# Performance work log

Measured on AMD Instinct MI355X. Metric: run time of the kernel, lower is better.

## Reference

```python
import jax, jax.numpy as jnp
import numpy as np

# Model config (matches init_kwargs)
D_MODEL = 512
D_STATE = 64
D_CONV = 4
EXPAND = 2
NHEADS = 16
HEADDIM = 64
D_INNER = EXPAND * D_MODEL          # 1024 == NHEADS * HEADDIM
D_IN_PROJ = 2 * D_INNER + 2 * D_STATE + NHEADS  # 2192
BATCH = 2
SEQLEN = 2048


def setup_inputs() -> dict:
    key = jax.random.key(0)
    ks = jax.random.split(key, 5)
    s = 0.02  # weight scale so activations stay well-conditioned
    return {
        "x": jax.random.normal(ks[0], (BATCH, SEQLEN, D_MODEL), jnp.float32),
        "W_in": jax.random.normal(ks[1], (D_IN_PROJ, D_MODEL), jnp.float32) * s,
        "conv_w": jax.random.normal(ks[2], (D_INNER, 1, D_CONV), jnp.float32) * 0.3,
        "conv_b": jnp.zeros((D_INNER,), jnp.float32),
        "A_log": jnp.zeros((NHEADS,), jnp.float32),       # torch init: log(ones)=0
        "dt_bias": jnp.ones((NHEADS,), jnp.float32),
        "W_out": jax.random.normal(ks[3], (D_MODEL, D_INNER), jnp.float32) * s,
    }


def reference(x, W_in, conv_w, conv_b, A_log, dt_bias, W_out):
    b, l, _ = x.shape
    # in_proj (no bias)
    proj = jnp.einsum('bld,ed->ble', x, W_in)  # [b, l, D_IN_PROJ]
    z, xs, B, C, dt = jnp.split(
        proj, [D_INNER, 2 * D_INNER, 2 * D_INNER + D_STATE, 2 * D_INNER + 2 * D_STATE], axis=-1)

    # depthwise causal conv1d: torch pads (d_conv-1) on both sides then truncates
    # right to seqlen, equivalent to left-padding by d_conv-1.
    xc = jax.lax.conv_general_dilated(
        xs.transpose(0, 2, 1), conv_w,
        window_strides=(1,), padding=[(D_CONV - 1, 0)],
        dimension_numbers=('NCH', 'OIH', 'NCH'),
        feature_group_count=D_INNER)
    xc = xc + conv_b[None, :, None]
    x_ssm = jax.nn.silu(xc).transpose(0, 2, 1)           # [b, l, D_INNER]
    xh = x_ssm.reshape(b, l, NHEADS, HEADDIM)            # [b, l, h, p]

    dt = jax.nn.softplus(dt + dt_bias)                   # [b, l, h]
    A = -jnp.exp(A_log)                                  # [h]
    dA = jnp.exp(dt * A)                                 # [b, l, h], in (0,1)

    # sequential selective scan over time (lax.scan), state h: [b, h, n, p]
    def step(h, inp):
        dAt, Bt, Ct, xt = inp                            # [b,h],[b,n],[b,n],[b,h,p]
        h = dAt[:, :, None, None] * h + jnp.einsum('bn,bhp->bhnp', Bt, xt)
        y = jnp.einsum('bn,bhnp->bhp', Ct, h)
        return h, y

    h0 = jnp.zeros((b, NHEADS, D_STATE, HEADDIM), x.dtype)
    _, ys = jax.lax.scan(step, h0, (dA.transpose(1, 0, 2),
                                    B.transpose(1, 0, 2),
                                    C.transpose(1, 0, 2),
                                    xh.transpose(1, 0, 2, 3)))
    y = ys.transpose(1, 0, 2, 3).reshape(b, l, D_INNER)  # [b, l, d_inner]

    y = y * jax.nn.silu(z)                               # gated output
    return jnp.einsum('ble,de->bld', y, W_out)           # out_proj (no bias)
```

## Files before the change

### kernel.cpp

```cpp
#include <hip/hip_runtime.h>
#include <cstdint>
#include <cstddef>

#define B_N     2
#define L_N     2048
#define DMODEL  512
#define DINNER  1024
#define DSTATE  64
#define NHEADS  16
#define EPROJ   2192
#define PB      2176
#define OFF_Z   0
#define OFF_XP  1024
#define OFF_B   2048
#define OFF_C   2112
#define LC      64
#define NC      32
#define MROWS   4096

typedef unsigned short u16;
typedef unsigned int   u32;
typedef __attribute__((ext_vector_type(8))) short short8;
typedef __attribute__((ext_vector_type(4))) float floatx4;

__device__ __forceinline__ float silu_f(float v) { return v / (1.f + __expf(-v)); }

__device__ __forceinline__ u16 f2bf(float f) {
    union { float f; uint32_t u; } v; v.f = f;
    uint32_t r = (v.u + 0x7FFFu + ((v.u >> 16) & 1u)) >> 16;
    return (u16)r;
}

__device__ __forceinline__ float bf2f(u16 b) {
    union { u32 u; float f; } v; v.u = (u32)b << 16; return v.f;
}

__device__ __forceinline__ u32 pack2(float lo, float hi) {
    return (u32)f2bf(lo) | ((u32)f2bf(hi) << 16);
}

__device__ __forceinline__ u32 cvtpk(float lo, float hi) {
    u32 r;
    asm("v_cvt_pk_bf16_f32 %0, %1, %2" : "=v"(r) : "v"(lo), "v"(hi));
    return r;
}

__device__ __forceinline__ uint4 pk8(const float4& a, const float4& b) {
    uint4 o;
    o.x = cvtpk(a.x, a.y); o.y = cvtpk(a.z, a.w);
    o.z = cvtpk(b.x, b.y); o.w = cvtpk(b.z, b.w);
    return o;
}

__device__ __forceinline__ float lane_bcast(float v, int n) {
    union { float f; uint32_t u; } a, b;
    a.f = v;
    b.u = __builtin_amdgcn_readlane(a.u, n);
    return b.f;
}

__device__ __forceinline__ short8 frag_ld(const u32* s, int row, int k0) {
    const u32* q = s + row * 33 + (k0 >> 1);
    union { u32 u[4]; short8 v; } r;
    r.u[0] = q[0]; r.u[1] = q[1]; r.u[2] = q[2]; r.u[3] = q[3];
    return r.v;
}

__device__ __forceinline__ void gload_lds16(const u16* g, u16* s) {
    __builtin_amdgcn_global_load_lds(
        (const __attribute__((address_space(1))) void*)g,
        (__attribute__((address_space(3))) void*)s,
        16, 0, 0);
}

template<int BM, int BN, int NPB, bool GUARD, bool PSPLIT, bool CVTIN,
         int NBX, int RBX, int RBY>
__global__ __launch_bounds__(256, 2) void gemm_mfma_bt(
    const void* __restrict__ Av, const void* __restrict__ Btv,
    float* __restrict__ Cf, u16* __restrict__ Cb, float* __restrict__ Dt,
    int M, int N, int K)
{
    constexpr int MI = BM / 32;
    constexpr int NI = BN / 32;
    constexpr int KB = 32 * NPB;
    constexpr int NGA = BM / 64;
    constexpr int NGB = (BN / 16 + 3) / 4;
    constexpr int XC  = NBX / RBX;
    __shared__ u16 As_[2][NPB][BM * 32];
    __shared__ u16 Bs_[2][NPB][BN * 32];

    const int tid = threadIdx.x;
    const int w   = tid >> 6;
    const int ln  = tid & 63;
    const int wm  = w >> 1, wn = w & 1;

    const int k  = blockIdx.x & 7;
    const int j  = blockIdx.x >> 3;
    const int bx = (k % XC) * RBX + (j % RBX);
    const int by = (k / XC) * RBY + (j / RBX);
    const int bm = by * BM;
    const int bn = bx * BN;

    const int srow = ln >> 2;
    const int skq  = (ln & 3) * 8;
    const int fr = ln & 15;
    const int fq = (ln >> 4) * 8;

    floatx4 acc[MI][NI];
    const floatx4 fzero = {0.f, 0.f, 0.f, 0.f};
    #pragma unroll
    for (int mi = 0; mi < MI; ++mi)
        #pragma unroll
        for (int ni = 0; ni < NI; ++ni) acc[mi][ni] = fzero;

    auto compute = [&](int buf) {
        #pragma unroll
        for (int p = 0; p < NPB; ++p) {
            short8 af[MI], bfv[NI];
            #pragma unroll
            for (int mi = 0; mi < MI; ++mi)
                af[mi] = *(const short8*)&As_[buf][p][(wm * (BM / 2) + mi * 16 + fr) * 32 + fq];
            #pragma unroll
            for (int ni = 0; ni < NI; ++ni)
                bfv[ni] = *(const short8*)&Bs_[buf][p][(wn * (BN / 2) + ni * 16 + fr) * 32 + fq];
            #pragma unroll
            for (int mi = 0; mi < MI; ++mi)
                #pragma unroll
                for (int ni = 0; ni < NI; ++ni)
                    acc[mi][ni] = __builtin_amdgcn_mfma_f32_16x16x32_bf16(
                        af[mi], bfv[ni], acc[mi][ni], 0, 0, 0);
        }
    };

    if constexpr (CVTIN) {
        const float* A  = (const float*)Av;
        const float* Bt = (const float*)Btv;
        float4 hA[NPB][NGA][2];
        float4 hB[NPB][NGB][2];

        auto ld = [&](int k0) {
            #pragma unroll
            for (int p = 0; p < NPB; ++p) {
                const int kp = k0 + p * 32;
                #pragma unroll
                for (int gi = 0; gi < NGA; ++gi) {
                    const int g = gi * 4 + w;
                    const float* s = A + (size_t)(bm + g * 16 + srow) * K + kp + skq;
                    hA[p][gi][0] = *(const float4*)s;
                    hA[p][gi][1] = *(const float4*)(s + 4);
                }
                #pragma unroll
                for (int gi = 0; gi < NGB; ++gi) {
                    const int g = gi * 4 + w;
                    if (g < BN / 16) {
                        int rn = bn + g * 16 + srow;
                        if (GUARD) rn = (rn < N) ? rn : (N - 1);
                        const float* s = Bt + (size_t)rn * K + kp + skq;
                        hB[p][gi][0] = *(const float4*)s;
                        hB[p][gi][1] = *(const float4*)(s + 4);
                    }
                }
            }
        };
        auto st = [&](int buf) {
            #pragma unroll
            for (int p = 0; p < NPB; ++p) {
                #pragma unroll
                for (int gi = 0; gi < NGA; ++gi) {
                    const int g = gi * 4 + w;
                    ((uint4*)&As_[buf][p][g * 16 * 32])[ln] =
                        pk8(hA[p][gi][0], hA[p][gi][1]);
                }
                #pragma unroll
                for (int gi = 0; gi < NGB; ++gi) {
                    const int g = gi * 4 + w;
                    if (g < BN / 16)
                        ((uint4*)&Bs_[buf][p][g * 16 * 32])[ln] =
                            pk8(hB[p][gi][0], hB[p][gi][1]);
                }
            }
        };

        ld(0); st(0);
        __syncthreads();
        int cur = 0;
        for (int k0 = 0; k0 + KB < K; k0 += KB) {
            ld(k0 + KB);
            compute(cur);
            st(cur ^ 1);
            __syncthreads();
            cur ^= 1;
        }
        compute(cur);
    } else {
        const u16* A  = (const u16*)Av;
        const u16* Bt = (const u16*)Btv;

        auto stage = [&](int buf, int k0) {
            #pragma unroll
            for (int p = 0; p < NPB; ++p) {
                const int kp = k0 + p * 32;
                #pragma unroll
                for (int g = 0; g < BM / 16; ++g) {
                    if ((g & 3) != w) continue;
                    gload_lds16(A + (size_t)(bm + g * 16 + srow) * K + kp + skq,
                                &As_[buf][p][g * 16 * 32]);
                }
                #pragma unroll
                for (int g = 0; g < BN / 16; ++g) {
                    if ((g & 3) != w) continue;
                    int rn = bn + g * 16 + srow;
                    if (GUARD) rn = (rn < N) ? rn : (N - 1);
                    gload_lds16(Bt + (size_t)rn * K + kp + skq,
                                &Bs_[buf][p][g * 16 * 32]);
                }
            }
        };

        stage(0, 0);
        __syncthreads();
        int cur = 0;
        for (int k0 = 0; k0 + KB < K; k0 += KB) {
            stage(cur ^ 1, k0 + KB);
            compute(cur);
            __syncthreads();
            cur ^= 1;
        }
        compute(cur);
    }

    const int cr = (ln >> 4) * 4;
    const int cc = ln & 15;
    #pragma unroll
    for (int mi = 0; mi < MI; ++mi) {
        const int row0 = bm + wm * (BM / 2) + mi * 16 + cr;
        #pragma unroll
        for (int ni = 0; ni < NI; ++ni) {
            const int col = bn + wn * (BN / 2) + ni * 16 + cc;
            #pragma unroll
            for (int r = 0; r < 4; ++r) {
                const int row = row0 + r;
                const float v = acc[mi][ni][r];
                if (PSPLIT) {
                    if (col < PB)
                        Cb[(size_t)row * PB + col] = f2bf(v);
                    else if (col < EPROJ)
                        Dt[(size_t)(col - PB) * MROWS + row] = v;
                } else {
                    Cf[(size_t)row * N + col] = v;
                }
            }
        }
    }
}

__global__ __launch_bounds__(256) void ssd_phase1(
    const u16* __restrict__ projb, const float* __restrict__ dtf,
    const float* __restrict__ cw, const float* __restrict__ cb,
    const float* __restrict__ A_log, const float* __restrict__ dt_bias,
    u16* __restrict__ hb, float* __restrict__ Pc, float* __restrict__ LaBuf,
    u32* __restrict__ xT)
{
    __shared__ u32 sBD[64 * 33];
    __shared__ u32 sXt[64 * 33];

    const int bid = blockIdx.x;
    const int c = bid & (NC - 1);
    const int h = (bid >> 5) & (NHEADS - 1);
    const int b = bid >> 9;
    const int tid = threadIdx.x;
    const int w = tid >> 6, ln = tid & 63;
    const int a = ln & 15, q = ln >> 4;
    const size_t r0 = (size_t)b * L_N + c * LC;

    float dt = dtf[(size_t)h * MROWS + r0 + ln] + dt_bias[h];
    float sp = (dt > 15.f) ? dt : log1pf(__expf(dt));
    float La = sp * (-__expf(A_log[h]));
    #pragma unroll
    for (int d = 1; d < 64; d <<= 1) {
        float up = __shfl_up(La, d, 64);
        if (ln >= d) La += up;
    }
    if (w == 0) LaBuf[(size_t)bid * 64 + ln] = La;
    const float La63 = lane_bcast(La, 63);

    const int ch = h * 64 + ln;
    const float4 w4 = *(const float4*)(cw + ch * 4);
    const float bias = cb[ch];
    const u16* xcol = projb + OFF_XP + ch;
    const size_t bbase = (size_t)b * L_N;

    float xr[3];
    #pragma unroll
    for (int i = 0; i < 3; ++i) {
        const int tl = c * LC + 16 * w - 3 + i;
        xr[i] = (tl >= 0) ? bf2f(xcol[(bbase + tl) * PB]) : 0.f;
    }

    #pragma unroll
    for (int j = 0; j < 8; ++j) {
        const int sp_ = w * 8 + j, s = sp_ * 2;
        const float xa = bf2f(xcol[(r0 + s) * PB]);
        const float xb = bf2f(xcol[(r0 + s + 1) * PB]);
        float a0 = bias, a1 = bias;
        a0 += xr[0] * w4.x; a0 += xr[1] * w4.y; a0 += xr[2] * w4.z; a0 += xa * w4.w;
        a1 += xr[1] * w4.x; a1 += xr[2] * w4.y; a1 += xa * w4.z;   a1 += xb * w4.w;
        xr[0] = xr[2]; xr[1] = xa; xr[2] = xb;
        const float x0 = silu_f(a0), x1 = silu_f(a1);
        const u32 xp = pack2(x0, x1);
        sXt[ln * 33 + sp_] = xp;
        xT[(size_t)bid * 2048 + sp_ * 64 + ln] = xp;
        const float w0 = __expf(La63 - lane_bcast(La, s));
        const float w1 = __expf(La63 - lane_bcast(La, s + 1));
        const float b0 = bf2f(projb[(r0 + s) * PB + OFF_B + ln]) * w0;
        const float b1 = bf2f(projb[(r0 + s + 1) * PB + OFF_B + ln]) * w1;
        sBD[ln * 33 + sp_] = pack2(b0, b1);
    }
    __syncthreads();

    short8 af[2], bf[4][2];
    #pragma unroll
    for (int ks = 0; ks < 2; ++ks)
        af[ks] = frag_ld(sBD, w * 16 + a, ks * 32 + q * 8);
    #pragma unroll
    for (int tn = 0; tn < 4; ++tn)
        #pragma unroll
        for (int ks = 0; ks < 2; ++ks)
            bf[tn][ks] = frag_ld(sXt, tn * 16 + a, ks * 32 + q * 8);

    const floatx4 fzero = {0.f, 0.f, 0.f, 0.f};
    floatx4 acc[4];
    #pragma unroll
    for (int tn = 0; tn < 4; ++tn) {
        acc[tn] = fzero;
        #pragma unroll
        for (int ks = 0; ks < 2; ++ks)
            acc[tn] = __builtin_amdgcn_mfma_f32_16x16x32_bf16(
                af[ks], bf[tn][ks], acc[tn], 0, 0, 0);
    }

    u16* hp = hb + (size_t)bid * 4096;
    #pragma unroll
    for (int tn = 0; tn < 4; ++tn)
        #pragma unroll
        for (int r = 0; r < 4; ++r)
            hp[(w * 16 + q * 4 + r) * 64 + tn * 16 + a] = f2bf(acc[tn][r]);
    if (tid == 0) Pc[bid] = __expf(La63);
}

__global__ __launch_bounds__(256) void ssd_phase2(
    u32* __restrict__ hb32, const float* __restrict__ Pc,
    const float* __restrict__ wsrc, u16* __restrict__ wdst, int nw)
{
    const int bid = blockIdx.x;
    if (bid >= 256) {
        const int i = (bid - 256) * 256 + threadIdx.x;
        if (i < nw) {
            float4 v = ((const float4*)wsrc)[i];
            ushort4 o;
            o.x = f2bf(v.x); o.y = f2bf(v.y); o.z = f2bf(v.z); o.w = f2bf(v.w);
            ((ushort4*)wdst)[i] = o;
        }
        return;
    }

    const int bh = bid >> 3;
    const int e = (bid & 7) * 256 + threadIdx.x;
    const size_t base = (size_t)(bh * NC) * 2048 + e;

    u32 v[NC];
    #pragma unroll
    for (int c = 0; c < NC; ++c)
        v[c] = hb32[base + (size_t)c * 2048];

    float c0 = 0.f, c1 = 0.f;
    #pragma unroll
    for (int c = 0; c < NC; ++c) {
        const u32 cur = v[c];
        const float lo = bf2f((u16)cur), hi = bf2f((u16)(cur >> 16));
        v[c] = pack2(c0, c1);
        const float Pv = Pc[bh * NC + c];
        c0 = fmaf(Pv, c0, lo);
        c1 = fmaf(Pv, c1, hi);
    }

    #pragma unroll
    for (int c = 0; c < NC; ++c)
        hb32[base + (size_t)c * 2048] = v[c];
}

__global__ __launch_bounds__(256) void ssd_phase3(
    const u16* __restrict__ projb, const u32* __restrict__ xT,
    const u16* __restrict__ hb, const float* __restrict__ LaBuf,
    u16* __restrict__ yz)
{
    __shared__ char lds[34048];
    u32* sBW   = (u32*)lds;
    u32* sC    = (u32*)(lds + 8448);
    u32* sXt   = (u32*)(lds + 16896);
    u32* sH    = (u32*)(lds + 25344);
    float* sLaF = (float*)(lds + 33792);
    float* sY  = (float*)(lds + 8448);

    const int bid = blockIdx.x;
    const int c = bid & (NC - 1);
    const int h = (bid >> 5) & (NHEADS - 1);
    const int b = bid >> 9;
    const int tid = threadIdx.x;
    const int w = tid >> 6, ln = tid & 63;
    const int a = ln & 15, q = ln >> 4;
    const int hw = ln >> 5, k32 = ln & 31;
    const size_t r0 = (size_t)b * L_N + c * LC;

    if (tid < 64) sLaF[tid] = LaBuf[(size_t)bid * 64 + tid];

    const u16* hs = hb + (size_t)bid * 4096;
    #pragma unroll
    for (int j = 0; j < 8; ++j) {
        const int rp = w * 8 + j;
        const int row = rp * 2 + hw;
        sBW[row * 33 + k32] = *(const u32*)(projb + (r0 + row) * PB + OFF_B + 2 * k32);
        sC [row * 33 + k32] = *(const u32*)(projb + (r0 + row) * PB + OFF_C + 2 * k32);
        sXt[ln * 33 + rp] = xT[(size_t)bid * 2048 + rp * 64 + ln];
        sH [ln * 33 + rp] = (u32)hs[(2 * rp) * 64 + ln]
                          | ((u32)hs[(2 * rp + 1) * 64 + ln] << 16);
    }
    __syncthreads();

    const floatx4 fzero = {0.f, 0.f, 0.f, 0.f};

    short8 cfr[2], bfr[4][2];
    #pragma unroll
    for (int ks = 0; ks < 2; ++ks)
        cfr[ks] = frag_ld(sC, w * 16 + a, ks * 32 + q * 8);
    #pragma unroll
    for (int tm = 0; tm < 4; ++tm)
        if (tm <= w)
            #pragma unroll
            for (int ks = 0; ks < 2; ++ks)
                bfr[tm][ks] = frag_ld(sBW, tm * 16 + a, ks * 32 + q * 8);
    floatx4 accS[4];
    #pragma unroll
    for (int tm = 0; tm < 4; ++tm) {
        if (tm > w) continue;
        accS[tm] = fzero;
        #pragma unroll
        for (int ks = 0; ks < 2; ++ks)
            accS[tm] = __builtin_amdgcn_mfma_f32_16x16x32_bf16(
                bfr[tm][ks], cfr[ks], accS[tm], 0, 0, 0);
    }
    __syncthreads();

    {
        const int i = w * 16 + a;
        const float Li = sLaF[i];
        #pragma unroll
        for (int tm = 0; tm < 4; ++tm) {
            const int d0 = i * 33 + tm * 8 + q * 2;
            if (tm > w) {
                sBW[d0] = 0; sBW[d0 + 1] = 0;
            } else {
                const float4 Ls = *(const float4*)(sLaF + tm * 16 + q * 4);
                float v[4];
                #pragma unroll
                for (int r = 0; r < 4; ++r) {
                    const int s = tm * 16 + q * 4 + r;
                    const float ww = (s <= i) ? __expf(Li - ((const float*)&Ls)[r]) : 0.f;
                    v[r] = accS[tm][r] * ww;
                }
                sBW[d0]     = pack2(v[0], v[1]);
                sBW[d0 + 1] = pack2(v[2], v[3]);
            }
        }
    }

    short8 hfr[4][2];
    #pragma unroll
    for (int tp = 0; tp < 4; ++tp)
        #pragma unroll
        for (int ks = 0; ks < 2; ++ks)
            hfr[tp][ks] = frag_ld(sH, tp * 16 + a, ks * 32 + q * 8);
    floatx4 accY[4];
    #pragma unroll
    for (int tp = 0; tp < 4; ++tp) {
        accY[tp] = fzero;
        #pragma unroll
        for (int ks = 0; ks < 2; ++ks)
            accY[tp] = __builtin_amdgcn_mfma_f32_16x16x32_bf16(
                cfr[ks], hfr[tp][ks], accY[tp], 0, 0, 0);
    }
    {
        const float4 Ls = *(const float4*)(sLaF + w * 16 + q * 4);
        float e4[4];
        #pragma unroll
        for (int r = 0; r < 4; ++r) e4[r] = __expf(((const float*)&Ls)[r]);
        #pragma unroll
        for (int tp = 0; tp < 4; ++tp)
            #pragma unroll
            for (int r = 0; r < 4; ++r) accY[tp][r] *= e4[r];
    }

    short8 wfr[2], xfr[4][2];
    #pragma unroll
    for (int ks = 0; ks < 2; ++ks)
        wfr[ks] = frag_ld(sBW, w * 16 + a, ks * 32 + q * 8);
    #pragma unroll
    for (int tp = 0; tp < 4; ++tp)
        #pragma unroll
        for (int ks = 0; ks < 2; ++ks)
            xfr[tp][ks] = frag_ld(sXt, tp * 16 + a, ks * 32 + q * 8);
    #pragma unroll
    for (int tp = 0; tp < 4; ++tp)
        #pragma unroll
        for (int ks = 0; ks < 2; ++ks)
            accY[tp] = __builtin_amdgcn_mfma_f32_16x16x32_bf16(
                wfr[ks], xfr[tp][ks], accY[tp], 0, 0, 0);
    __syncthreads();

    #pragma unroll
    for (int tp = 0; tp < 4; ++tp)
        #pragma unroll
        for (int r = 0; r < 4; ++r)
            sY[(w * 16 + q * 4 + r) * 66 + tp * 16 + a] = accY[tp][r];
    #pragma unroll
    for (int ii = 0; ii < 16; ++ii) {
        const int i = w * 16 + ii;
        const float y = sY[i * 66 + ln];
        const float z = bf2f(projb[(r0 + i) * PB + OFF_Z + h * 64 + ln]);
        yz[(r0 + i) * DINNER + h * 64 + ln] = f2bf(y * silu_f(z));
    }
}

extern "C" void kernel_launch(void* const* d_in, const int* in_sizes, int n_in,
                              void* d_out, int out_size, void* d_ws, size_t ws_size,
                              hipStream_t stream)
{
    const float* x       = (const float*)d_in[0];
    const float* W_in    = (const float*)d_in[1];
    const float* conv_w  = (const float*)d_in[2];
    const float* conv_b  = (const float*)d_in[3];
    const float* A_log   = (const float*)d_in[4];
    const float* dt_bias = (const float*)d_in[5];
    const float* W_out   = (const float*)d_in[6];
    float* out = (float*)d_out;

    u16*   projb = (u16*)d_ws;
    float* dtf   = (float*)(projb + (size_t)4096 * PB);
    u16*   hb    = (u16*)(dtf + (size_t)4096 * 16);
    float* Pc    = (float*)(hb + (size_t)1024 * 4096);
    float* LaBuf = Pc + 1024;
    u16*   xbf   = (u16*)(LaBuf + 1024 * 64);
    u16*   wibf  = xbf + (size_t)4096 * DMODEL;
    u16*   wobf  = wibf + (size_t)EPROJ * DMODEL;
    u16*   yzbf  = wobf + (size_t)DMODEL * DINNER;
    u32*   xT    = (u32*)(yzbf + (size_t)4096 * DINNER);

    const int M = B_N * L_N;
    const int n2 = DMODEL * DINNER / 4;

    gemm_mfma_bt<128, 160, 2, true, true, true, 14, 7, 8>
        <<<dim3(14 * (M / 128)), 256, 0, stream>>>(
        x, W_in, nullptr, projb, dtf, M, EPROJ, DMODEL);

    ssd_phase1<<<B_N * NHEADS * NC, 256, 0, stream>>>(
        projb, dtf, conv_w, conv_b, A_log, dt_bias, hb, Pc, LaBuf, xT);
    ssd_phase2<<<256 + (n2 + 255) / 256, 256, 0, stream>>>(
        (u32*)hb, Pc, W_out, wobf, n2);
    ssd_phase3<<<B_N * NHEADS * NC, 256, 0, stream>>>(
        projb, xT, hb, LaBuf, yzbf);

    gemm_mfma_bt<64, 64, 4, false, false, false, 8, 8, 8>
        <<<dim3((DMODEL / 64) * (M / 64)), 256, 0, stream>>>(
        yzbf, wobf, out, nullptr, nullptr, M, DMODEL, DINNER);
}
```

Baseline: 131.1 us.

## Drop chunk-state scan kernel; recompute prefix states in phase3 and convert W_out inline

Removes the separate inter-chunk state propagation kernel (phase2). Each phase3 block now rebuilds its incoming state by summing all earlier chunk states, weighted by the cumulative decay products. The W_out fp32-to-bf16 conversion that phase2 also did is moved into the output GEMM through a new mixed mode: A is staged as bf16 directly into LDS, and B is loaded as fp32 and packed on the fly. This saves one launch and a round trip through the state buffer. In exchange, phase3 blocks for later chunks do O(c) state reads, which makes the work quadratic in chunk count and unbalanced across blocks.

```diff
diff --git a/kernel.cpp b/kernel.cpp
--- a/kernel.cpp
+++ b/kernel.cpp
@@ -73,7 +73,7 @@
         16, 0, 0);
 }
 
-template<int BM, int BN, int NPB, bool GUARD, bool PSPLIT, bool CVTIN,
+template<int BM, int BN, int NPB, bool GUARD, bool PSPLIT, int CVM,
          int NBX, int RBX, int RBY>
 __global__ __launch_bounds__(256, 2) void gemm_mfma_bt(
     const void* __restrict__ Av, const void* __restrict__ Btv,
@@ -132,7 +132,7 @@
         }
     };
 
-    if constexpr (CVTIN) {
+    if constexpr (CVM == 1) {
         const float* A  = (const float*)Av;
         const float* Bt = (const float*)Btv;
         float4 hA[NPB][NGA][2];
@@ -192,6 +192,64 @@
             cur ^= 1;
         }
         compute(cur);
+    } else if constexpr (CVM == 2) {
+        const u16*   A  = (const u16*)Av;
+        const float* Bt = (const float*)Btv;
+        float4 hB[NPB][NGB][2];
+
+        auto stgA = [&](int buf, int k0) {
+            #pragma unroll
+            for (int p = 0; p < NPB; ++p) {
+                const int kp = k0 + p * 32;
+                #pragma unroll
+                for (int g = 0; g < BM / 16; ++g) {
+                    if ((g & 3) != w) continue;
+                    gload_lds16(A + (size_t)(bm + g * 16 + srow) * K + kp + skq,
+                                &As_[buf][p][g * 16 * 32]);
+                }
+            }
+        };
+        auto ldB = [&](int k0) {
+            #pragma unroll
+            for (int p = 0; p < NPB; ++p) {
+                const int kp = k0 + p * 32;
+                #pragma unroll
+                for (int gi = 0; gi < NGB; ++gi) {
+                    const int g = gi * 4 + w;
+                    if (g < BN / 16) {
+                        int rn = bn + g * 16 + srow;
+                        if (GUARD) rn = (rn < N) ? rn : (N - 1);
+                        const float* s = Bt + (size_t)rn * K + kp + skq;
+                        hB[p][gi][0] = *(const float4*)s;
+                        hB[p][gi][1] = *(const float4*)(s + 4);
+                    }
+                }
+            }
+        };
+        auto stB = [&](int buf) {
+            #pragma unroll
+            for (int p = 0; p < NPB; ++p)
+                #pragma unroll
+                for (int gi = 0; gi < NGB; ++gi) {
+                    const int g = gi * 4 + w;
+                    if (g < BN / 16)
+                        ((uint4*)&Bs_[buf][p][g * 16 * 32])[ln] =
+                            pk8(hB[p][gi][0], hB[p][gi][1]);
+                }
+        };
+
+        ldB(0); stgA(0, 0); stB(0);
+        __syncthreads();
+        int cur = 0;
+        for (int k0 = 0; k0 + KB < K; k0 += KB) {
+            ldB(k0 + KB);
+            stgA(cur ^ 1, k0 + KB);
+            compute(cur);
+            stB(cur ^ 1);
+            __syncthreads();
+            cur ^= 1;
+        }
+        compute(cur);
     } else {
         const u16* A  = (const u16*)Av;
         const u16* Bt = (const u16*)Btv;
@@ -258,7 +316,7 @@
     const u16* __restrict__ projb, const float* __restrict__ dtf,
     const float* __restrict__ cw, const float* __restrict__ cb,
     const float* __restrict__ A_log, const float* __restrict__ dt_bias,
-    u16* __restrict__ hb, float* __restrict__ Pc, float* __restrict__ LaBuf,
+    u32* __restrict__ hb2, float* __restrict__ Pc, float* __restrict__ LaBuf,
     u32* __restrict__ xT)
 {
     __shared__ u32 sBD[64 * 33];
@@ -339,60 +397,20 @@
                 af[ks], bf[tn][ks], acc[tn], 0, 0, 0);
     }
 
-    u16* hp = hb + (size_t)bid * 4096;
-    #pragma unroll
-    for (int tn = 0; tn < 4; ++tn)
-        #pragma unroll
-        for (int r = 0; r < 4; ++r)
-            hp[(w * 16 + q * 4 + r) * 64 + tn * 16 + a] = f2bf(acc[tn][r]);
+    u32* hp = hb2 + (size_t)bid * 2048;
+    const int np0 = w * 8 + q * 2;
+    #pragma unroll
+    for (int tn = 0; tn < 4; ++tn) {
+        hp[(np0    ) * 64 + tn * 16 + a] = pack2(acc[tn][0], acc[tn][1]);
+        hp[(np0 + 1) * 64 + tn * 16 + a] = pack2(acc[tn][2], acc[tn][3]);
+    }
     if (tid == 0) Pc[bid] = __expf(La63);
-}
-
-__global__ __launch_bounds__(256) void ssd_phase2(
-    u32* __restrict__ hb32, const float* __restrict__ Pc,
-    const float* __restrict__ wsrc, u16* __restrict__ wdst, int nw)
-{
-    const int bid = blockIdx.x;
-    if (bid >= 256) {
-        const int i = (bid - 256) * 256 + threadIdx.x;
-        if (i < nw) {
-            float4 v = ((const float4*)wsrc)[i];
-            ushort4 o;
-            o.x = f2bf(v.x); o.y = f2bf(v.y); o.z = f2bf(v.z); o.w = f2bf(v.w);
-            ((ushort4*)wdst)[i] = o;
-        }
-        return;
-    }
-
-    const int bh = bid >> 3;
-    const int e = (bid & 7) * 256 + threadIdx.x;
-    const size_t base = (size_t)(bh * NC) * 2048 + e;
-
-    u32 v[NC];
-    #pragma unroll
-    for (int c = 0; c < NC; ++c)
-        v[c] = hb32[base + (size_t)c * 2048];
-
-    float c0 = 0.f, c1 = 0.f;
-    #pragma unroll
-    for (int c = 0; c < NC; ++c) {
-        const u32 cur = v[c];
-        const float lo = bf2f((u16)cur), hi = bf2f((u16)(cur >> 16));
-        v[c] = pack2(c0, c1);
-        const float Pv = Pc[bh * NC + c];
-        c0 = fmaf(Pv, c0, lo);
-        c1 = fmaf(Pv, c1, hi);
-    }
-
-    #pragma unroll
-    for (int c = 0; c < NC; ++c)
-        hb32[base + (size_t)c * 2048] = v[c];
 }
 
 __global__ __launch_bounds__(256) void ssd_phase3(
     const u16* __restrict__ projb, const u32* __restrict__ xT,
-    const u16* __restrict__ hb, const float* __restrict__ LaBuf,
-    u16* __restrict__ yz)
+    const u32* __restrict__ hb2, const float* __restrict__ Pc,
+    const float* __restrict__ LaBuf, u16* __restrict__ yz)
 {
     __shared__ char lds[34048];
     u32* sBW   = (u32*)lds;
@@ -414,7 +432,25 @@
 
     if (tid < 64) sLaF[tid] = LaBuf[(size_t)bid * 64 + tid];
 
-    const u16* hs = hb + (size_t)bid * 4096;
+    float hacc[8][2];
+    #pragma unroll
+    for (int jj = 0; jj < 8; ++jj) { hacc[jj][0] = 0.f; hacc[jj][1] = 0.f; }
+    {
+        const u32* hb_bh = hb2 + (size_t)(bid - c) * 2048;
+        const float* Pbh = Pc + (bid - c);
+        float wgt = 1.f;
+        for (int cp = c - 1; cp >= 0; --cp) {
+            const u32* hc = hb_bh + (size_t)cp * 2048;
+            #pragma unroll
+            for (int jj = 0; jj < 8; ++jj) {
+                const u32 v = hc[(w * 8 + jj) * 64 + ln];
+                hacc[jj][0] = fmaf(wgt, bf2f((u16)v), hacc[jj][0]);
+                hacc[jj][1] = fmaf(wgt, bf2f((u16)(v >> 16)), hacc[jj][1]);
+            }
+            wgt *= Pbh[cp];
+        }
+    }
+
     #pragma unroll
     for (int j = 0; j < 8; ++j) {
         const int rp = w * 8 + j;
@@ -422,8 +458,7 @@
         sBW[row * 33 + k32] = *(const u32*)(projb + (r0 + row) * PB + OFF_B + 2 * k32);
         sC [row * 33 + k32] = *(const u32*)(projb + (r0 + row) * PB + OFF_C + 2 * k32);
         sXt[ln * 33 + rp] = xT[(size_t)bid * 2048 + rp * 64 + ln];
-        sH [ln * 33 + rp] = (u32)hs[(2 * rp) * 64 + ln]
-                          | ((u32)hs[(2 * rp + 1) * 64 + ln] << 16);
+        sH [ln * 33 + rp] = pack2(hacc[j][0], hacc[j][1]);
     }
     __syncthreads();
 
@@ -546,30 +581,24 @@
 
     u16*   projb = (u16*)d_ws;
     float* dtf   = (float*)(projb + (size_t)4096 * PB);
-    u16*   hb    = (u16*)(dtf + (size_t)4096 * 16);
-    float* Pc    = (float*)(hb + (size_t)1024 * 4096);
+    u32*   hb2   = (u32*)(dtf + (size_t)4096 * 16);
+    float* Pc    = (float*)(hb2 + (size_t)1024 * 2048);
     float* LaBuf = Pc + 1024;
-    u16*   xbf   = (u16*)(LaBuf + 1024 * 64);
-    u16*   wibf  = xbf + (size_t)4096 * DMODEL;
-    u16*   wobf  = wibf + (size_t)EPROJ * DMODEL;
-    u16*   yzbf  = wobf + (size_t)DMODEL * DINNER;
+    u16*   yzbf  = (u16*)(LaBuf + 1024 * 64);
     u32*   xT    = (u32*)(yzbf + (size_t)4096 * DINNER);
 
     const int M = B_N * L_N;
-    const int n2 = DMODEL * DINNER / 4;
-
-    gemm_mfma_bt<128, 160, 2, true, true, true, 14, 7, 8>
+
+    gemm_mfma_bt<128, 160, 2, true, true, 1, 14, 7, 8>
         <<<dim3(14 * (M / 128)), 256, 0, stream>>>(
         x, W_in, nullptr, projb, dtf, M, EPROJ, DMODEL);
 
     ssd_phase1<<<B_N * NHEADS * NC, 256, 0, stream>>>(
-        projb, dtf, conv_w, conv_b, A_log, dt_bias, hb, Pc, LaBuf, xT);
-    ssd_phase2<<<256 + (n2 + 255) / 256, 256, 0, stream>>>(
-        (u32*)hb, Pc, W_out, wobf, n2);
+        projb, dtf, conv_w, conv_b, A_log, dt_bias, hb2, Pc, LaBuf, xT);
     ssd_phase3<<<B_N * NHEADS * NC, 256, 0, stream>>>(
-        projb, xT, hb, LaBuf, yzbf);
-
-    gemm_mfma_bt<64, 64, 4, false, false, false, 8, 8, 8>
+        projb, xT, hb2, Pc, LaBuf, yzbf);
+
+    gemm_mfma_bt<64, 64, 4, false, false, 2, 8, 8, 8>
         <<<dim3((DMODEL / 64) * (M / 64)), 256, 0, stream>>>(
-        yzbf, wobf, out, nullptr, nullptr, M, DMODEL, DINNER);
-}
+        yzbf, W_out, out, nullptr, nullptr, M, DMODEL, DINNER);
+}
```

Measured after the change: 146.5 us. 11.7% more time.
